# Kernel tuning notes

Measured on AMD Instinct MI355X. Metric: run time of the kernel, lower is better.

The kernel has to match this reference:

```python
import jax, jax.numpy as jnp
import numpy as np

SR = 44100
B, T = 4, SR * 3          # batch, samples (duration_secs=3)
NWT, L = 64, 512          # n_wavetables, wavetable_len


def setup_inputs() -> dict:
    key = jax.random.key(0)
    k1, k2, k3, k4, k5 = jax.random.split(key, 5)
    pitch = jax.random.uniform(k1, (B, T, 1), dtype=jnp.float32, minval=50.0, maxval=500.0)
    amplitude = jax.random.uniform(k2, (B, T, 1), dtype=jnp.float32)
    y = jax.random.normal(k3, (B, T), dtype=jnp.float32)
    wavetables = jax.random.normal(k4, (NWT, L), dtype=jnp.float32) * 0.01
    # replicate init: last sample equals first sample of each table
    wavetables = wavetables.at[:, -1].set(wavetables[:, 0])
    conv_w = jax.random.normal(k5, (1, 1, 5), dtype=jnp.float32) * 0.3  # Conv1d(1,1,5)
    conv_b = jnp.zeros((1,), dtype=jnp.float32)
    return {"pitch": pitch, "amplitude": amplitude, "y": y,
            "wavetables": wavetables, "conv_w": conv_w, "conv_b": conv_b,
            "duration_secs": 3}


def reference(pitch, amplitude, y, wavetables, conv_w, conv_b, duration_secs):
    Lwt = wavetables.shape[1]
    freq = pitch.squeeze(-1)                                   # (B, T)
    increment = freq / SR * Lwt                                # (B, T)
    # NOTE: faithful to source: subtract batch-row 0 from every row
    index = jnp.cumsum(increment, axis=1) - increment[0]
    index = index % Lwt
    idx_low = jnp.floor(index)
    idx_high = jnp.ceil(index)
    alpha = index - idx_low                                    # (B, T)
    il = idx_low.astype(jnp.int32)
    ih = idx_high.astype(jnp.int32) % Lwt
    # vectorized over all 64 wavetables at once (source loops in Python)
    low = jnp.take(wavetables, il, axis=1)                     # (N, B, T)
    high = jnp.take(wavetables, ih, axis=1)                    # (N, B, T)
    waveforms = low + alpha * (high - low)                     # (N, B, T)
    # attention: mean over batch of waveform * y
    att = jnp.mean(waveforms * y, axis=1)                      # (N, T)
    att = jax.lax.conv_general_dilated(
        att[:, None, :], conv_w, window_strides=(1,), padding=[(2, 2)],
        dimension_numbers=("NCH", "OIH", "NCH"))[:, 0, :] + conv_b[0]
    att = jax.nn.softmax(att, axis=0)                          # softmax over wavetables
    out = jnp.einsum("nbt,nt->bt", waveforms, att)             # (B, T)
    out = out[..., None] * amplitude                           # (B, T, 1)
    return out
```

## Files before the change

### kernel.cpp

```cpp
#include <hip/hip_runtime.h>
#include <math.h>

#define LWT 512
#define NWT 64
#define BB 4
#define SBASE 16
#define BLK 32
#define HALO 36


#define INC_C ((float)(512.0 / 44100.0))

__device__ __forceinline__ float inc_mul(float p) {
  float v = p * INC_C;
  asm volatile("" : "+v"(v));
  return v;
}
__device__ __forceinline__ float inc_of(const float* p, int t) { return inc_mul(p[t]); }

__device__ __forceinline__ float wt_at(const float* wtT, unsigned byteoff) {
  return *reinterpret_cast<const float*>(reinterpret_cast<const char*>(wtT) + byteoff);
}

__global__ void __launch_bounds__(256) scan_level0(const float* __restrict__ pitch,
                                                   float* __restrict__ sarr,
                                                   float* __restrict__ s1g,
                                                   const float* __restrict__ wt,
                                                   float* __restrict__ wtT,
                                                   int T, int NB1) {
  if (blockIdx.y == BB) {
    int i = blockIdx.x * blockDim.x + threadIdx.x;
    if (i < NWT * LWT) {
      int n = i >> 9, c = i & 511;
      wtT[c * NWT + n] = wt[i];
    }
    return;
  }
  int k = blockIdx.x * blockDim.x + threadIdx.x;
  int b = blockIdx.y;
  if (k >= NB1) return;
  const float* prow = pitch + (size_t)b * T;
  float* srow = sarr + (size_t)b * T;
  int t0 = k * SBASE;
  float run = 0.0f;
  if (t0 + SBASE <= T) {
    const float4* p4 = reinterpret_cast<const float4*>(prow + t0);
    float4* s4o = reinterpret_cast<float4*>(srow + t0);
#pragma unroll
    for (int i = 0; i < 4; ++i) {
      float4 v = p4[i];
      float4 o;
      run += inc_mul(v.x); o.x = run;
      run += inc_mul(v.y); o.y = run;
      run += inc_mul(v.z); o.z = run;
      run += inc_mul(v.w); o.w = run;
      s4o[i] = o;
    }
  } else {
    for (int t = t0; t < T; ++t) { run += inc_of(prow, t); srow[t] = run; }
  }
  s1g[(size_t)b * NB1 + k] = run;
}

__global__ void __launch_bounds__(256) scan_level1(float* __restrict__ s1g,
                                                   float* __restrict__ s2g,
                                                   int NB1, int NB2) {
  int k = blockIdx.x * blockDim.x + threadIdx.x;
  int b = blockIdx.y;
  if (k >= NB2) return;
  float* s1r = s1g + (size_t)b * NB1;
  int a0 = k * SBASE, a1 = a0 + SBASE < NB1 ? a0 + SBASE : NB1;
  float run = 0.0f;
  for (int a = a0; a < a1; ++a) { run += s1r[a]; s1r[a] = run; }
  s2g[(size_t)b * NB2 + k] = run;
}

__global__ void __launch_bounds__(256) scan_upper(float* __restrict__ s2g, int NB2) {
  __shared__ float s2[BB][544];
  __shared__ float s3[BB][48];
  __shared__ float s4[BB][16];
  int tid = threadIdx.x;
  const int NB3 = (NB2 + SBASE - 1) / SBASE;
  const int NB4 = (NB3 + SBASE - 1) / SBASE;
  for (int b = 0; b < BB; ++b)
    for (int a = tid; a < NB2; a += 256) s2[b][a] = s2g[(size_t)b * NB2 + a];
  __syncthreads();
  if (tid < BB * NB3) {
    int b = tid / NB3, k = tid % NB3;
    int a0 = k * SBASE, a1 = a0 + SBASE < NB2 ? a0 + SBASE : NB2;
    float run = 0.0f;
    for (int a = a0; a < a1; ++a) { run += s2[b][a]; s2[b][a] = run; }
    s3[b][k] = run;
  }
  __syncthreads();
  if (tid < BB * NB4) {
    int b = tid / NB4, k = tid % NB4;
    int a0 = k * SBASE, a1 = a0 + SBASE < NB3 ? a0 + SBASE : NB3;
    float run = 0.0f;
    for (int a = a0; a < a1; ++a) { run += s3[b][a]; s3[b][a] = run; }
    s4[b][k] = run;
  }
  __syncthreads();
  if (tid < BB) {
    int b = tid;
    float r = 0.0f;
    for (int a = 0; a < NB4; ++a) { r += s4[b][a]; s4[b][a] = r; }
  }
  __syncthreads();
  if (tid < BB * NB3) {
    int b = tid / NB3, a = tid % NB3;
    if (a >= SBASE) s3[b][a] = s3[b][a] + s4[b][a / SBASE - 1];
  }
  __syncthreads();
  for (int b = 0; b < BB; ++b)
    for (int a = tid; a < NB2; a += 256) {
      float v = s2[b][a];
      if (a >= SBASE) v = v + s3[b][a / SBASE - 1];
      s2g[(size_t)b * NB2 + a] = v;
    }
}

__device__ __forceinline__ float dpp_reduce_add(float x) {
  x += __int_as_float(__builtin_amdgcn_update_dpp(0, __float_as_int(x), 0xB1, 0xf, 0xf, true));
  x += __int_as_float(__builtin_amdgcn_update_dpp(0, __float_as_int(x), 0x4E, 0xf, 0xf, true));
  x += __int_as_float(__builtin_amdgcn_update_dpp(0, __float_as_int(x), 0x141, 0xf, 0xf, true));
  x += __int_as_float(__builtin_amdgcn_update_dpp(0, __float_as_int(x), 0x140, 0xf, 0xf, true));
  x += __int_as_float(__builtin_amdgcn_update_dpp(0, __float_as_int(x), 0x142, 0xa, 0xf, true));
  x += __int_as_float(__builtin_amdgcn_update_dpp(0, __float_as_int(x), 0x143, 0xc, 0xf, true));
  return __int_as_float(__builtin_amdgcn_readlane(__float_as_int(x), 63));
}

__global__ void __launch_bounds__(256) fused_out(
    const float* __restrict__ pitch, const float* __restrict__ sarr,
    const float* __restrict__ s1g, const float* __restrict__ s2g,
    const float* __restrict__ y, const float* __restrict__ amp,
    const float* __restrict__ wtT, const float* __restrict__ cw,
    const float* __restrict__ cb, float* __restrict__ out,
    int T, int NB1, int NB2) {
  __shared__ float lds_att[HALO][64];
  __shared__ unsigned ilo_l[BB][HALO];
  __shared__ unsigned ihi_l[BB][HALO];
  __shared__ float alf_l[BB][HALO];
  __shared__ float y_l[BB][HALO];
  __shared__ float amp_l[BB][HALO];
  __shared__ float out_l[BB][BLK + 1];
  int t0 = blockIdx.x * BLK;
  int wid = threadIdx.x >> 6, lane = threadIdx.x & 63;
  unsigned lane4 = (unsigned)lane << 2;

  {
    int b = wid;
    for (int i = lane; i < HALO; i += 64) {
      int t = t0 - 2 + i;
      if (t >= 0 && t < T) {
        float S = sarr[(size_t)b * T + t];
        if (t >= SBASE) {
          int k1 = (t >> 4) - 1;
          float s1v = s1g[b * NB1 + k1];
          if (k1 >= SBASE) s1v = s1v + s2g[b * NB2 + (k1 >> 4) - 1];
          S = S + s1v;
        }
        float iv = S - inc_of(pitch, t);
        float q = iv * (1.0f / 512.0f);
        float k = floorf(q);
        iv = fmaf(-k, 512.0f, iv);
        float fl = floorf(iv);
        float alpha = iv - fl;
        int ili = (int)fl; if (ili > 511) ili = 511;
        int ihi = ((int)ceilf(iv)) & 511;
        ilo_l[b][i] = (unsigned)ili << 8;
        ihi_l[b][i] = (unsigned)ihi << 8;
        alf_l[b][i] = alpha;
        y_l[b][i] = y[(size_t)b * T + t];
        amp_l[b][i] = amp[(size_t)b * T + t];
      }
    }
  }
  __syncthreads();

  for (int i = wid; i < HALO; i += 4) {
    int t = t0 - 2 + i;
    float acc = 0.0f;
    if (t >= 0 && t < T) {
#pragma unroll
      for (int b = 0; b < BB; ++b) {
        float lo = wt_at(wtT, ilo_l[b][i] + lane4);
        float hi = wt_at(wtT, ihi_l[b][i] + lane4);
        float alpha = alf_l[b][i];
        acc += (lo + alpha * (hi - lo)) * y_l[b][i];
      }
      acc *= 0.25f;
    }
    lds_att[i][lane] = acc;
  }
  __syncthreads();

  float w0 = cw[0], w1 = cw[1], w2 = cw[2], w3 = cw[3], w4 = cw[4];
  float bias = cb[0];
#pragma unroll 4
  for (int i = wid; i < BLK; i += 4) {
    int t = t0 + i;
    if (t >= T) continue;
    float c = bias + lds_att[i][lane] * w0 + lds_att[i + 1][lane] * w1 +
              lds_att[i + 2][lane] * w2 + lds_att[i + 3][lane] * w3 +
              lds_att[i + 4][lane] * w4;
    float e = __expf(c);
    float r0, r1, r2, r3;
    {
      float lo = wt_at(wtT, ilo_l[0][i + 2] + lane4);
      float hi = wt_at(wtT, ihi_l[0][i + 2] + lane4);
      r0 = e * (lo + alf_l[0][i + 2] * (hi - lo));
    }
    {
      float lo = wt_at(wtT, ilo_l[1][i + 2] + lane4);
      float hi = wt_at(wtT, ihi_l[1][i + 2] + lane4);
      r1 = e * (lo + alf_l[1][i + 2] * (hi - lo));
    }
    {
      float lo = wt_at(wtT, ilo_l[2][i + 2] + lane4);
      float hi = wt_at(wtT, ihi_l[2][i + 2] + lane4);
      r2 = e * (lo + alf_l[2][i + 2] * (hi - lo));
    }
    {
      float lo = wt_at(wtT, ilo_l[3][i + 2] + lane4);
      float hi = wt_at(wtT, ihi_l[3][i + 2] + lane4);
      r3 = e * (lo + alf_l[3][i + 2] * (hi - lo));
    }
    float s0 = dpp_reduce_add(r0);
    float s1_ = dpp_reduce_add(r1);
    float s2_ = dpp_reduce_add(r2);
    float s3_ = dpp_reduce_add(r3);
    float ssum = dpp_reduce_add(e);
#if __has_builtin(__builtin_amdgcn_rcpf)
    float rc = __builtin_amdgcn_rcpf(ssum);
#else
    float rc = 1.0f / ssum;
#endif
    if (lane < BB) {
      float pv = lane == 0 ? s0 : lane == 1 ? s1_ : lane == 2 ? s2_ : s3_;
      out_l[lane][i] = pv * rc * amp_l[lane][i + 2];
    }
  }
  __syncthreads();

  {
    int b = wid;
    int t = t0 + lane;
    if (lane < BLK && t < T) out[(size_t)b * T + t] = out_l[b][lane];
  }
}

extern "C" void kernel_launch(void* const* d_in, const int* in_sizes, int n_in,
                              void* d_out, int out_size, void* d_ws, size_t ws_size,
                              hipStream_t stream) {
  const float* pitch = (const float*)d_in[0];
  const float* amp   = (const float*)d_in[1];
  const float* y     = (const float*)d_in[2];
  const float* wt    = (const float*)d_in[3];
  const float* cw    = (const float*)d_in[4];
  const float* cb    = (const float*)d_in[5];
  float* out = (float*)d_out;

  int BT = in_sizes[2];
  int T = BT / BB;
  int NB1 = (T + SBASE - 1) / SBASE;
  int NB2 = (NB1 + SBASE - 1) / SBASE;

  float* ws   = (float*)d_ws;
  float* sarr = ws;
  float* wtT  = ws + (size_t)BT;
  float* s1g  = ws + (size_t)BT + NWT * LWT;
  float* s2g  = s1g + (size_t)BB * NB1;

  hipLaunchKernelGGL(scan_level0, dim3(128, BB + 1), dim3(256), 0, stream,
                     pitch, sarr, s1g, wt, wtT, T, NB1);
  hipLaunchKernelGGL(scan_level1, dim3((NB2 + 255) / 256, BB), dim3(256), 0, stream,
                     s1g, s2g, NB1, NB2);
  hipLaunchKernelGGL(scan_upper, dim3(1), dim3(256), 0, stream, s2g, NB2);
  hipLaunchKernelGGL(fused_out, dim3((T + BLK - 1) / BLK), dim3(256), 0, stream,
                     pitch, sarr, s1g, s2g, y, amp, wtT, cw, cb, out, T, NB1, NB2);
}
```

Before: 55.71 us.

## Pack wavetable as (value, delta) pairs and merge mid-level scan kernels

Precomputes each wavetable entry as a float2 (lo, hi-lo) in transposed layout, so each interpolation is one 8-byte gather plus an fma instead of two separate 4-byte gathers. This removes the ihi shared array and the ceil computation. Separately, it merges scan_level1 and scan_upper into a single per-batch scan_mid kernel with 1024 threads, dropping one kernel launch. The cost is twice the wavetable footprint in the workspace, and the mid-level scan now runs on only four blocks.

```diff
diff --git a/kernel.cpp b/kernel.cpp
--- a/kernel.cpp
+++ b/kernel.cpp
@@ -18,21 +18,23 @@
 }
 __device__ __forceinline__ float inc_of(const float* p, int t) { return inc_mul(p[t]); }
 
-__device__ __forceinline__ float wt_at(const float* wtT, unsigned byteoff) {
-  return *reinterpret_cast<const float*>(reinterpret_cast<const char*>(wtT) + byteoff);
+__device__ __forceinline__ float2 wt_at2(const float2* wtP, unsigned byteoff) {
+  return *reinterpret_cast<const float2*>(reinterpret_cast<const char*>(wtP) + byteoff);
 }
 
 __global__ void __launch_bounds__(256) scan_level0(const float* __restrict__ pitch,
                                                    float* __restrict__ sarr,
                                                    float* __restrict__ s1g,
                                                    const float* __restrict__ wt,
-                                                   float* __restrict__ wtT,
+                                                   float2* __restrict__ wtP,
                                                    int T, int NB1) {
   if (blockIdx.y == BB) {
-    int i = blockIdx.x * blockDim.x + threadIdx.x;
-    if (i < NWT * LWT) {
-      int n = i >> 9, c = i & 511;
-      wtT[c * NWT + n] = wt[i];
+    int idx = blockIdx.x * blockDim.x + threadIdx.x;
+    if (idx < NWT * LWT) {
+      int n = idx >> 9, c = idx & 511;
+      float lo = wt[n * 512 + c];
+      float hi = wt[n * 512 + ((c + 1) & 511)];
+      wtP[c * NWT + n] = make_float2(lo, hi - lo);
     }
     return;
   }
@@ -62,62 +64,46 @@
   s1g[(size_t)b * NB1 + k] = run;
 }
 
-__global__ void __launch_bounds__(256) scan_level1(float* __restrict__ s1g,
-                                                   float* __restrict__ s2g,
-                                                   int NB1, int NB2) {
-  int k = blockIdx.x * blockDim.x + threadIdx.x;
-  int b = blockIdx.y;
-  if (k >= NB2) return;
+__global__ void __launch_bounds__(1024) scan_mid(float* __restrict__ s1g,
+                                                 float* __restrict__ s2g,
+                                                 int NB1, int NB2) {
+  int b = blockIdx.x, tid = threadIdx.x;
   float* s1r = s1g + (size_t)b * NB1;
-  int a0 = k * SBASE, a1 = a0 + SBASE < NB1 ? a0 + SBASE : NB1;
-  float run = 0.0f;
-  for (int a = a0; a < a1; ++a) { run += s1r[a]; s1r[a] = run; }
-  s2g[(size_t)b * NB2 + k] = run;
-}
-
-__global__ void __launch_bounds__(256) scan_upper(float* __restrict__ s2g, int NB2) {
-  __shared__ float s2[BB][544];
-  __shared__ float s3[BB][48];
-  __shared__ float s4[BB][16];
-  int tid = threadIdx.x;
+  __shared__ float s2[544];
+  __shared__ float s3[48];
+  __shared__ float s4[16];
   const int NB3 = (NB2 + SBASE - 1) / SBASE;
   const int NB4 = (NB3 + SBASE - 1) / SBASE;
-  for (int b = 0; b < BB; ++b)
-    for (int a = tid; a < NB2; a += 256) s2[b][a] = s2g[(size_t)b * NB2 + a];
-  __syncthreads();
-  if (tid < BB * NB3) {
-    int b = tid / NB3, k = tid % NB3;
-    int a0 = k * SBASE, a1 = a0 + SBASE < NB2 ? a0 + SBASE : NB2;
+  if (tid < NB2) {
+    int a0 = tid * SBASE, a1 = a0 + SBASE < NB1 ? a0 + SBASE : NB1;
     float run = 0.0f;
-    for (int a = a0; a < a1; ++a) { run += s2[b][a]; s2[b][a] = run; }
-    s3[b][k] = run;
-  }
-  __syncthreads();
-  if (tid < BB * NB4) {
-    int b = tid / NB4, k = tid % NB4;
-    int a0 = k * SBASE, a1 = a0 + SBASE < NB3 ? a0 + SBASE : NB3;
+    for (int a = a0; a < a1; ++a) { run += s1r[a]; s1r[a] = run; }
+    s2[tid] = run;
+  }
+  __syncthreads();
+  if (tid < NB3) {
+    int a0 = tid * SBASE, a1 = a0 + SBASE < NB2 ? a0 + SBASE : NB2;
     float run = 0.0f;
-    for (int a = a0; a < a1; ++a) { run += s3[b][a]; s3[b][a] = run; }
-    s4[b][k] = run;
-  }
-  __syncthreads();
-  if (tid < BB) {
-    int b = tid;
-    float r = 0.0f;
-    for (int a = 0; a < NB4; ++a) { r += s4[b][a]; s4[b][a] = r; }
-  }
-  __syncthreads();
-  if (tid < BB * NB3) {
-    int b = tid / NB3, a = tid % NB3;
-    if (a >= SBASE) s3[b][a] = s3[b][a] + s4[b][a / SBASE - 1];
-  }
-  __syncthreads();
-  for (int b = 0; b < BB; ++b)
-    for (int a = tid; a < NB2; a += 256) {
-      float v = s2[b][a];
-      if (a >= SBASE) v = v + s3[b][a / SBASE - 1];
-      s2g[(size_t)b * NB2 + a] = v;
-    }
+    for (int a = a0; a < a1; ++a) { run += s2[a]; s2[a] = run; }
+    s3[tid] = run;
+  }
+  __syncthreads();
+  if (tid < NB4) {
+    int a0 = tid * SBASE, a1 = a0 + SBASE < NB3 ? a0 + SBASE : NB3;
+    float run = 0.0f;
+    for (int a = a0; a < a1; ++a) { run += s3[a]; s3[a] = run; }
+    s4[tid] = run;
+  }
+  __syncthreads();
+  if (tid == 0) { float r = 0.0f; for (int a = 0; a < NB4; ++a) { r += s4[a]; s4[a] = r; } }
+  __syncthreads();
+  if (tid < NB3 && tid >= SBASE) s3[tid] = s3[tid] + s4[tid / SBASE - 1];
+  __syncthreads();
+  if (tid < NB2) {
+    float v = s2[tid];
+    if (tid >= SBASE) v = v + s3[tid / SBASE - 1];
+    s2g[(size_t)b * NB2 + tid] = v;
+  }
 }
 
 __device__ __forceinline__ float dpp_reduce_add(float x) {
@@ -134,19 +120,18 @@
     const float* __restrict__ pitch, const float* __restrict__ sarr,
     const float* __restrict__ s1g, const float* __restrict__ s2g,
     const float* __restrict__ y, const float* __restrict__ amp,
-    const float* __restrict__ wtT, const float* __restrict__ cw,
+    const float2* __restrict__ wtP, const float* __restrict__ cw,
     const float* __restrict__ cb, float* __restrict__ out,
     int T, int NB1, int NB2) {
   __shared__ float lds_att[HALO][64];
   __shared__ unsigned ilo_l[BB][HALO];
-  __shared__ unsigned ihi_l[BB][HALO];
   __shared__ float alf_l[BB][HALO];
   __shared__ float y_l[BB][HALO];
   __shared__ float amp_l[BB][HALO];
   __shared__ float out_l[BB][BLK + 1];
   int t0 = blockIdx.x * BLK;
   int wid = threadIdx.x >> 6, lane = threadIdx.x & 63;
-  unsigned lane4 = (unsigned)lane << 2;
+  unsigned lane8 = (unsigned)lane << 3;
 
   {
     int b = wid;
@@ -167,9 +152,7 @@
         float fl = floorf(iv);
         float alpha = iv - fl;
         int ili = (int)fl; if (ili > 511) ili = 511;
-        int ihi = ((int)ceilf(iv)) & 511;
-        ilo_l[b][i] = (unsigned)ili << 8;
-        ihi_l[b][i] = (unsigned)ihi << 8;
+        ilo_l[b][i] = (unsigned)ili << 9;
         alf_l[b][i] = alpha;
         y_l[b][i] = y[(size_t)b * T + t];
         amp_l[b][i] = amp[(size_t)b * T + t];
@@ -184,10 +167,9 @@
     if (t >= 0 && t < T) {
 #pragma unroll
       for (int b = 0; b < BB; ++b) {
-        float lo = wt_at(wtT, ilo_l[b][i] + lane4);
-        float hi = wt_at(wtT, ihi_l[b][i] + lane4);
-        float alpha = alf_l[b][i];
-        acc += (lo + alpha * (hi - lo)) * y_l[b][i];
+        float2 p = wt_at2(wtP, ilo_l[b][i] + lane8);
+        float wv = fmaf(alf_l[b][i], p.y, p.x);
+        acc += wv * y_l[b][i];
       }
       acc *= 0.25f;
     }
@@ -205,27 +187,14 @@
               lds_att[i + 2][lane] * w2 + lds_att[i + 3][lane] * w3 +
               lds_att[i + 4][lane] * w4;
     float e = __expf(c);
-    float r0, r1, r2, r3;
-    {
-      float lo = wt_at(wtT, ilo_l[0][i + 2] + lane4);
-      float hi = wt_at(wtT, ihi_l[0][i + 2] + lane4);
-      r0 = e * (lo + alf_l[0][i + 2] * (hi - lo));
-    }
-    {
-      float lo = wt_at(wtT, ilo_l[1][i + 2] + lane4);
-      float hi = wt_at(wtT, ihi_l[1][i + 2] + lane4);
-      r1 = e * (lo + alf_l[1][i + 2] * (hi - lo));
-    }
-    {
-      float lo = wt_at(wtT, ilo_l[2][i + 2] + lane4);
-      float hi = wt_at(wtT, ihi_l[2][i + 2] + lane4);
-      r2 = e * (lo + alf_l[2][i + 2] * (hi - lo));
-    }
-    {
-      float lo = wt_at(wtT, ilo_l[3][i + 2] + lane4);
-      float hi = wt_at(wtT, ihi_l[3][i + 2] + lane4);
-      r3 = e * (lo + alf_l[3][i + 2] * (hi - lo));
-    }
+    float2 p0 = wt_at2(wtP, ilo_l[0][i + 2] + lane8);
+    float2 p1 = wt_at2(wtP, ilo_l[1][i + 2] + lane8);
+    float2 p2 = wt_at2(wtP, ilo_l[2][i + 2] + lane8);
+    float2 p3 = wt_at2(wtP, ilo_l[3][i + 2] + lane8);
+    float r0 = e * fmaf(alf_l[0][i + 2], p0.y, p0.x);
+    float r1 = e * fmaf(alf_l[1][i + 2], p1.y, p1.x);
+    float r2 = e * fmaf(alf_l[2][i + 2], p2.y, p2.x);
+    float r3 = e * fmaf(alf_l[3][i + 2], p3.y, p3.x);
     float s0 = dpp_reduce_add(r0);
     float s1_ = dpp_reduce_add(r1);
     float s2_ = dpp_reduce_add(r2);
@@ -268,15 +237,13 @@
 
   float* ws   = (float*)d_ws;
   float* sarr = ws;
-  float* wtT  = ws + (size_t)BT;
-  float* s1g  = ws + (size_t)BT + NWT * LWT;
+  float2* wtP = (float2*)(ws + (size_t)BT);
+  float* s1g  = ws + (size_t)BT + 2 * NWT * LWT;
   float* s2g  = s1g + (size_t)BB * NB1;
 
   hipLaunchKernelGGL(scan_level0, dim3(128, BB + 1), dim3(256), 0, stream,
-                     pitch, sarr, s1g, wt, wtT, T, NB1);
-  hipLaunchKernelGGL(scan_level1, dim3((NB2 + 255) / 256, BB), dim3(256), 0, stream,
-                     s1g, s2g, NB1, NB2);
-  hipLaunchKernelGGL(scan_upper, dim3(1), dim3(256), 0, stream, s2g, NB2);
+                     pitch, sarr, s1g, wt, wtP, T, NB1);
+  hipLaunchKernelGGL(scan_mid, dim3(BB), dim3(1024), 0, stream, s1g, s2g, NB1, NB2);
   hipLaunchKernelGGL(fused_out, dim3((T + BLK - 1) / BLK), dim3(256), 0, stream,
-                     pitch, sarr, s1g, s2g, y, amp, wtT, cw, cb, out, T, NB1, NB2);
-}
+                     pitch, sarr, s1g, s2g, y, amp, wtP, cw, cb, out, T, NB1, NB2);
+}
```

After: 60.44 us. 8.5% more time.
